# Performance work log

Hardware: AMD Instinct MI355X
Metric: run time of the kernel (lower is better)

The kernel has to match this reference:

```python
import jax, jax.numpy as jnp
import numpy as np

INPUT_SIZE = 1024
HIDDEN_SIZE = 1024
BATCH = 32
SEQ = 512


def setup_inputs() -> dict:
    key = jax.random.key(0)
    ks = jax.random.split(key, 20)
    stdv = 1.0 / np.sqrt(HIDDEN_SIZE)

    def u(k, shape):
        return jax.random.uniform(k, shape, jnp.float32, -stdv, stdv)

    inp = {
        'inputs': jax.random.normal(ks[0], (BATCH, SEQ, INPUT_SIZE), jnp.float32),
        'h0': jax.random.normal(ks[1], (1, BATCH, HIDDEN_SIZE), jnp.float32),
        'c0': jax.random.normal(ks[2], (1, BATCH, HIDDEN_SIZE), jnp.float32),
    }
    names = ['ii', 'hi', 'if_', 'hf', 'io', 'ho', 'ig', 'hg']
    kidx = 3
    for n in names:
        in_dim = INPUT_SIZE if n[0] == 'i' and n not in ('hi', 'hf', 'ho', 'hg') else HIDDEN_SIZE
        inp['w_' + n] = u(ks[kidx], (HIDDEN_SIZE, in_dim)); kidx += 1
        inp['b_' + n] = u(ks[kidx], (HIDDEN_SIZE, 1)); kidx += 1
    return inp


def _gate(x, h0s, w_i, b_i, w_h, b_h):
    # x: [B,T,I]; h0s: [B,H]; w_i: [H,I]; w_h: [H,H]; biases [H,1]
    z = (jnp.einsum('bti,hi->bth', x, w_i)
         + (h0s @ w_h.T)[:, None, :]
         + b_i[:, 0] + b_h[:, 0])
    return z


def reference(inputs, h0, c0,
              w_ii, b_ii, w_hi, b_hi,
              w_if_, b_if_, w_hf, b_hf,
              w_io, b_io, w_ho, b_ho,
              w_ig, b_ig, w_hg, b_hg):
    # Faithful to source: h_t/c_t are NEVER updated inside the time loop
    # (original code omits the reassignment), so all timesteps use the
    # initial state -> fully vectorizable over T.
    h0s = h0[0]  # [B,H]
    c0s = c0[0]  # [B,H]
    i = jax.nn.sigmoid(_gate(inputs, h0s, w_ii, b_ii, w_hi, b_hi))
    f = jax.nn.sigmoid(_gate(inputs, h0s, w_if_, b_if_, w_hf, b_hf))
    g = jnp.tanh(_gate(inputs, h0s, w_ig, b_ig, w_hg, b_hg))
    o = jax.nn.sigmoid(_gate(inputs, h0s, w_io, b_io, w_ho, b_ho))
    c_next = f * c0s[:, None, :] + i * g          # [B,T,H]
    h_next = o * jnp.tanh(c_next)                 # [B,T,H]
    hidden_seq = jnp.transpose(h_next, (1, 0, 2))  # [T,B,H] (torch cat over dim 0)
    h_last = hidden_seq[-1][None]                  # [1,B,H]
    c_last = c_next[:, -1][None]                   # [1,B,H]
    return hidden_seq, h_last, c_last
```

## Files before the change

kernel.cpp:

```cpp
#include <hip/hip_runtime.h>
#include <hip/hip_bf16.h>

#define HSEQ 16777216
#define NH 1024

typedef __attribute__((ext_vector_type(8))) short bf16x8;
typedef __attribute__((ext_vector_type(4))) float f32x4;

__device__ __forceinline__ unsigned short f2bf(float f) {
  unsigned u = __builtin_bit_cast(unsigned, f);
  u += 0x7fffu + ((u >> 16) & 1u);
  return (unsigned short)(u >> 16);
}

__global__ __launch_bounds__(256) void cvt_all(
    const float* __restrict__ x,
    const float* __restrict__ wi, const float* __restrict__ wf,
    const float* __restrict__ wo, const float* __restrict__ wg,
    unsigned short* __restrict__ xb, unsigned short* __restrict__ wb) {
  int bid = blockIdx.x;
  const float* src; unsigned short* dst; int base, iters;
  if (bid < 2048) {
    src = x; dst = xb; base = bid * 8192; iters = 8;
  } else {
    int g = bid - 2048; int ws = g >> 8; int blk = g & 255;
    src = (ws == 0) ? wi : (ws == 1) ? wf : (ws == 2) ? wo : wg;
    dst = wb + ws * 1048576; base = blk * 4096; iters = 4;
  }
  int t = threadIdx.x;
  for (int i = 0; i < iters; ++i) {
    int idx = base + i * 1024 + t * 4;
    float4 v = *reinterpret_cast<const float4*>(src + idx);
    ushort4 o;
    o.x = f2bf(v.x); o.y = f2bf(v.y); o.z = f2bf(v.z); o.w = f2bf(v.w);
    *reinterpret_cast<ushort4*>(dst + idx) = o;
  }
}

__global__ __launch_bounds__(256) void hz_kernel(
    const float* __restrict__ h0,
    const float* __restrict__ wh_i, const float* __restrict__ wh_f,
    const float* __restrict__ wh_o, const float* __restrict__ wh_g,
    const float* __restrict__ bi_i, const float* __restrict__ bh_i,
    const float* __restrict__ bi_f, const float* __restrict__ bh_f,
    const float* __restrict__ bi_o, const float* __restrict__ bh_o,
    const float* __restrict__ bi_g, const float* __restrict__ bh_g,
    float* __restrict__ hz) {
  __shared__ float ws[8 * 1024];
  int g = blockIdx.x >> 7;
  int hb = blockIdx.x & 127;
  const float* wh = (g == 0) ? wh_i : (g == 1) ? wh_f : (g == 2) ? wh_o : wh_g;
  const float* bi = (g == 0) ? bi_i : (g == 1) ? bi_f : (g == 2) ? bi_o : bi_g;
  const float* bh = (g == 0) ? bh_i : (g == 1) ? bh_f : (g == 2) ? bh_o : bh_g;
  int tid = threadIdx.x;
  const float4* wsrc = reinterpret_cast<const float4*>(wh + hb * 8 * 1024);
  float4* wdst = reinterpret_cast<float4*>(ws);
  for (int i = tid; i < 2048; i += 256) wdst[i] = wsrc[i];
  __syncthreads();
  int b = tid & 31;
  int hh = tid >> 5;
  const float4* hv = reinterpret_cast<const float4*>(h0 + b * NH);
  const float4* wv = reinterpret_cast<const float4*>(ws + hh * NH);
  float acc = 0.f;
  for (int k = 0; k < 256; ++k) {
    float4 a = hv[k], w4 = wv[k];
    acc += a.x * w4.x + a.y * w4.y + a.z * w4.z + a.w * w4.w;
  }
  int h = hb * 8 + hh;
  hz[g * (32 * NH) + b * NH + h] = acc + bi[h] + bh[h];
}

__device__ __forceinline__ void load_lds16(const void* gsrc, void* lds) {
  __builtin_amdgcn_global_load_lds(
      (const __attribute__((address_space(1))) unsigned int*)gsrc,
      (__attribute__((address_space(3))) unsigned int*)lds, 16, 0, 0);
}

__global__ __launch_bounds__(512, 2) void lstm_gemm8(
    const unsigned short* __restrict__ xb,
    const unsigned short* __restrict__ wb,
    const float* __restrict__ hz,
    const float* __restrict__ c0,
    float* __restrict__ out) {
  __shared__ unsigned short As[2][16384];
  __shared__ unsigned short Bs[2][16384];

  const int bid0 = blockIdx.x;
  const int bid = (bid0 & 7) * 128 + (bid0 >> 3);
  const int ht = bid & 15;
  const int mt = bid >> 4;
  const int mBase = mt * 256;
  const int hBase = ht * 64;

  const int tid = threadIdx.x;
  const int lane = tid & 63;
  const int w = tid >> 6;
  const int wr = w >> 2;
  const int wc = w & 3;
  const int laneLow = lane & 15;
  const int lane4 = lane >> 4;
  const int lx = lane & 7;

  const int sRow = w * 8 + (lane >> 3);
  const int sCol = ((lane & 7) ^ (lane >> 3)) * 8;

#define STAGE_A(buf, kt, h)                                                        \
  do {                                                                             \
    int k0_ = (kt) * 64;                                                           \
    _Pragma("unroll") for (int r_ = 0; r_ < 2; ++r_) {                             \
      load_lds16(xb + (size_t)(mBase + (h) * 128 + r_ * 64 + sRow) * 1024 + k0_ + sCol, \
                 &As[buf][(h) * 8192 + r_ * 4096 + w * 512]);                      \
    }                                                                              \
  } while (0)

#define STAGE_B(buf, kt, h)                                                        \
  do {                                                                             \
    int k0_ = (kt) * 64;                                                           \
    _Pragma("unroll") for (int r_ = 0; r_ < 2; ++r_) {                             \
      load_lds16(wb + (size_t)((h) * 2 + r_) * 1048576 +                           \
                     (size_t)(hBase + sRow) * 1024 + k0_ + sCol,                   \
                 &Bs[buf][(h) * 8192 + r_ * 4096 + w * 512]);                      \
    }                                                                              \
  } while (0)

#define LDA(buf, mh)                                                               \
  do {                                                                             \
    _Pragma("unroll") for (int mi = 0; mi < 4; ++mi)                               \
    _Pragma("unroll") for (int kk = 0; kk < 2; ++kk) {                             \
      int row_ = wr * 128 + (mh) * 64 + mi * 16 + laneLow;                         \
      int slot_ = (kk * 4 + lane4) ^ lx;                                           \
      af[mi][kk] = *reinterpret_cast<const bf16x8*>(&As[buf][row_ * 64 + slot_ * 8]); \
    }                                                                              \
  } while (0)

#define LDB(buf, qh)                                                               \
  do {                                                                             \
    _Pragma("unroll") for (int q = 0; q < 2; ++q)                                  \
    _Pragma("unroll") for (int kk = 0; kk < 2; ++kk) {                             \
      int row_ = ((qh) * 2 + q) * 64 + wc * 16 + laneLow;                          \
      int slot_ = (kk * 4 + lane4) ^ lx;                                           \
      bq[q][kk] = *reinterpret_cast<const bf16x8*>(&Bs[buf][row_ * 64 + slot_ * 8]); \
    }                                                                              \
  } while (0)

#define DO_MFMA(MH, QH)                                                            \
  do {                                                                             \
    __builtin_amdgcn_s_setprio(1);                                                 \
    _Pragma("unroll") for (int mi = 0; mi < 4; ++mi)                               \
    _Pragma("unroll") for (int q = 0; q < 2; ++q)                                  \
    _Pragma("unroll") for (int kk = 0; kk < 2; ++kk)                               \
      acc[(MH) * 4 + mi][(QH) * 2 + q] = __builtin_amdgcn_mfma_f32_16x16x32_bf16(  \
          af[mi][kk], bq[q][kk], acc[(MH) * 4 + mi][(QH) * 2 + q], 0, 0, 0);       \
    __builtin_amdgcn_s_setprio(0);                                                 \
  } while (0)

#define BARRIER __builtin_amdgcn_s_barrier()
#define WAIT_LGKM0 asm volatile("s_waitcnt lgkmcnt(0)" ::: "memory")

  f32x4 acc[8][4];
#pragma unroll
  for (int i = 0; i < 8; ++i)
#pragma unroll
    for (int j = 0; j < 4; ++j) acc[i][j] = (f32x4){0.f, 0.f, 0.f, 0.f};

  STAGE_B(0, 0, 0); STAGE_B(0, 0, 1);
  STAGE_A(0, 0, 0); STAGE_A(0, 0, 1);
  STAGE_B(1, 1, 0);
  asm volatile("s_waitcnt vmcnt(2)" ::: "memory");
  BARRIER;

  bf16x8 af[4][2], bq[2][2];

  for (int it = 0; it < 8; ++it) {
    const int t1 = 2 * it + 1;
    const int t2 = (2 * it + 2 > 15) ? 15 : 2 * it + 2;
    const int t3 = (2 * it + 3 > 15) ? 15 : 2 * it + 3;

    LDA(0, 0); LDB(0, 0);
    STAGE_B(1, t1, 1); STAGE_A(1, t1, 0);
    BARRIER; WAIT_LGKM0; DO_MFMA(0, 0); BARRIER;

    LDB(0, 1);
    STAGE_A(1, t1, 1);
    BARRIER; WAIT_LGKM0; DO_MFMA(0, 1); BARRIER;

    LDA(0, 1); LDB(0, 0);
    BARRIER; WAIT_LGKM0; DO_MFMA(1, 0); BARRIER;

    LDB(0, 1);
    STAGE_B(0, t2, 0); STAGE_A(0, t2, 0);
    asm volatile("s_waitcnt vmcnt(4)" ::: "memory");
    BARRIER; WAIT_LGKM0; DO_MFMA(1, 1); BARRIER;

    LDA(1, 0); LDB(1, 0);
    STAGE_B(0, t2, 1);
    BARRIER; WAIT_LGKM0; DO_MFMA(0, 0); BARRIER;

    LDB(1, 1);
    STAGE_A(0, t2, 1);
    BARRIER; WAIT_LGKM0; DO_MFMA(0, 1); BARRIER;

    LDA(1, 1); LDB(1, 0);
    BARRIER; WAIT_LGKM0; DO_MFMA(1, 0); BARRIER;

    LDB(1, 1);
    STAGE_B(1, t3, 0);
    asm volatile("s_waitcnt vmcnt(2)" ::: "memory");
    BARRIER; WAIT_LGKM0; DO_MFMA(1, 1); BARRIER;
  }

  const int b = mBase >> 9;
  const int h = hBase + wc * 16 + laneLow;
  float hzv[4];
#pragma unroll
  for (int g = 0; g < 4; ++g) hzv[g] = hz[g * 32768 + b * NH + h];
  const float c0v = c0[b * NH + h];
#pragma unroll
  for (int mi16 = 0; mi16 < 8; ++mi16) {
#pragma unroll
    for (int r = 0; r < 4; ++r) {
      int m = mBase + wr * 128 + mi16 * 16 + lane4 * 4 + r;
      int t = m & 511;
      float zi = acc[mi16][0][r] + hzv[0];
      float zf = acc[mi16][1][r] + hzv[1];
      float zo = acc[mi16][2][r] + hzv[2];
      float zg = acc[mi16][3][r] + hzv[3];
      float iv = 1.f / (1.f + __expf(-zi));
      float fv = 1.f / (1.f + __expf(-zf));
      float ov = 1.f / (1.f + __expf(-zo));
      float gv = tanhf(zg);
      float cv = fv * c0v + iv * gv;
      float hval = ov * tanhf(cv);
      out[(size_t)t * 32768 + b * NH + h] = hval;
      if (t == 511) {
        out[HSEQ + b * NH + h] = hval;
        out[HSEQ + 32768 + b * NH + h] = cv;
      }
    }
  }
}

extern "C" void kernel_launch(void* const* d_in, const int* in_sizes, int n_in,
                              void* d_out, int out_size, void* d_ws, size_t ws_size,
                              hipStream_t stream) {
  const float* x    = (const float*)d_in[0];
  const float* h0   = (const float*)d_in[1];
  const float* c0   = (const float*)d_in[2];
  const float* w_ii = (const float*)d_in[3];
  const float* b_ii = (const float*)d_in[4];
  const float* w_hi = (const float*)d_in[5];
  const float* b_hi = (const float*)d_in[6];
  const float* w_if = (const float*)d_in[7];
  const float* b_if = (const float*)d_in[8];
  const float* w_hf = (const float*)d_in[9];
  const float* b_hf = (const float*)d_in[10];
  const float* w_io = (const float*)d_in[11];
  const float* b_io = (const float*)d_in[12];
  const float* w_ho = (const float*)d_in[13];
  const float* b_ho = (const float*)d_in[14];
  const float* w_ig = (const float*)d_in[15];
  const float* b_ig = (const float*)d_in[16];
  const float* w_hg = (const float*)d_in[17];
  const float* b_hg = (const float*)d_in[18];

  unsigned short* xb = (unsigned short*)d_ws;
  unsigned short* wb = xb + 16777216;
  float* hz = (float*)(wb + 4 * 1048576);
  float* out = (float*)d_out;

  hipLaunchKernelGGL(cvt_all, dim3(3072), dim3(256), 0, stream,
                     x, w_ii, w_if, w_io, w_ig, xb, wb);
  hipLaunchKernelGGL(hz_kernel, dim3(512), dim3(256), 0, stream, h0,
                     w_hi, w_hf, w_ho, w_hg,
                     b_ii, b_hi, b_if, b_hf, b_io, b_ho, b_ig, b_hg, hz);
  hipLaunchKernelGGL(lstm_gemm8, dim3(1024), dim3(512), 0, stream, xb, wb, hz, c0, out);
}
```

Before: 257.4 us.

## Double-buffer LDS fragment registers to overlap loads with MFMA in GEMM loop

Restructures the main K loop so LDS-to-register fragment loads for the next MFMA block go into alternate register sets (afX/afY, bqA/bqB) while the current MFMA block runs. This removes the per-phase lgkmcnt(0) waits and halves the barriers. Global staging addresses are also precomputed as 32-bit offsets to cut address arithmetic. The cost is extra VGPR pressure and a more fragile hand-ordered schedule of buffer reuse across barriers.

```diff
diff --git a/kernel.cpp b/kernel.cpp
--- a/kernel.cpp
+++ b/kernel.cpp
@@ -103,59 +103,58 @@
 
   const int sRow = w * 8 + (lane >> 3);
   const int sCol = ((lane & 7) ^ (lane >> 3)) * 8;
+  const unsigned aStage = (unsigned)((mBase + sRow) * 1024 + sCol);
+  const unsigned bStage = (unsigned)((hBase + sRow) * 1024 + sCol);
 
 #define STAGE_A(buf, kt, h)                                                        \
   do {                                                                             \
-    int k0_ = (kt) * 64;                                                           \
     _Pragma("unroll") for (int r_ = 0; r_ < 2; ++r_) {                             \
-      load_lds16(xb + (size_t)(mBase + (h) * 128 + r_ * 64 + sRow) * 1024 + k0_ + sCol, \
+      load_lds16(xb + aStage + (unsigned)(((h) * 128 + r_ * 64) * 1024 + (kt) * 64), \
                  &As[buf][(h) * 8192 + r_ * 4096 + w * 512]);                      \
     }                                                                              \
   } while (0)
 
 #define STAGE_B(buf, kt, h)                                                        \
   do {                                                                             \
-    int k0_ = (kt) * 64;                                                           \
     _Pragma("unroll") for (int r_ = 0; r_ < 2; ++r_) {                             \
-      load_lds16(wb + (size_t)((h) * 2 + r_) * 1048576 +                           \
-                     (size_t)(hBase + sRow) * 1024 + k0_ + sCol,                   \
+      load_lds16(wb + bStage + (unsigned)(((h) * 2 + r_) * 1048576 + (kt) * 64),   \
                  &Bs[buf][(h) * 8192 + r_ * 4096 + w * 512]);                      \
     }                                                                              \
   } while (0)
 
-#define LDA(buf, mh)                                                               \
+#define LDA(dst, buf, mh)                                                          \
   do {                                                                             \
     _Pragma("unroll") for (int mi = 0; mi < 4; ++mi)                               \
     _Pragma("unroll") for (int kk = 0; kk < 2; ++kk) {                             \
       int row_ = wr * 128 + (mh) * 64 + mi * 16 + laneLow;                         \
       int slot_ = (kk * 4 + lane4) ^ lx;                                           \
-      af[mi][kk] = *reinterpret_cast<const bf16x8*>(&As[buf][row_ * 64 + slot_ * 8]); \
-    }                                                                              \
-  } while (0)
-
-#define LDB(buf, qh)                                                               \
+      dst[mi][kk] = *reinterpret_cast<const bf16x8*>(&As[buf][row_ * 64 + slot_ * 8]); \
+    }                                                                              \
+  } while (0)
+
+#define LDB(dst, buf, qh)                                                          \
   do {                                                                             \
     _Pragma("unroll") for (int q = 0; q < 2; ++q)                                  \
     _Pragma("unroll") for (int kk = 0; kk < 2; ++kk) {                             \
       int row_ = ((qh) * 2 + q) * 64 + wc * 16 + laneLow;                          \
       int slot_ = (kk * 4 + lane4) ^ lx;                                           \
-      bq[q][kk] = *reinterpret_cast<const bf16x8*>(&Bs[buf][row_ * 64 + slot_ * 8]); \
-    }                                                                              \
-  } while (0)
-
-#define DO_MFMA(MH, QH)                                                            \
+      dst[q][kk] = *reinterpret_cast<const bf16x8*>(&Bs[buf][row_ * 64 + slot_ * 8]); \
+    }                                                                              \
+  } while (0)
+
+#define MFMA16(A, B, MH, QH)                                                       \
   do {                                                                             \
     __builtin_amdgcn_s_setprio(1);                                                 \
     _Pragma("unroll") for (int mi = 0; mi < 4; ++mi)                               \
     _Pragma("unroll") for (int q = 0; q < 2; ++q)                                  \
     _Pragma("unroll") for (int kk = 0; kk < 2; ++kk)                               \
       acc[(MH) * 4 + mi][(QH) * 2 + q] = __builtin_amdgcn_mfma_f32_16x16x32_bf16(  \
-          af[mi][kk], bq[q][kk], acc[(MH) * 4 + mi][(QH) * 2 + q], 0, 0, 0);       \
+          A[mi][kk], B[q][kk], acc[(MH) * 4 + mi][(QH) * 2 + q], 0, 0, 0);         \
     __builtin_amdgcn_s_setprio(0);                                                 \
   } while (0)
 
-#define BARRIER __builtin_amdgcn_s_barrier()
-#define WAIT_LGKM0 asm volatile("s_waitcnt lgkmcnt(0)" ::: "memory")
+#define BAR __builtin_amdgcn_s_barrier()
+#define VM(n) asm volatile("s_waitcnt vmcnt(" #n ")" ::: "memory")
 
   f32x4 acc[8][4];
 #pragma unroll
@@ -163,50 +162,61 @@
 #pragma unroll
     for (int j = 0; j < 4; ++j) acc[i][j] = (f32x4){0.f, 0.f, 0.f, 0.f};
 
-  STAGE_B(0, 0, 0); STAGE_B(0, 0, 1);
-  STAGE_A(0, 0, 0); STAGE_A(0, 0, 1);
-  STAGE_B(1, 1, 0);
-  asm volatile("s_waitcnt vmcnt(2)" ::: "memory");
-  BARRIER;
-
-  bf16x8 af[4][2], bq[2][2];
+  bf16x8 afX[4][2], afY[4][2], bqA[2][2], bqB[2][2];
+
+  STAGE_B(0, 0, 0); STAGE_B(0, 0, 1); STAGE_A(0, 0, 0); STAGE_A(0, 0, 1);
+  STAGE_B(1, 1, 0); STAGE_B(1, 1, 1); STAGE_A(1, 1, 0);
+  VM(0);
+  BAR;
+  LDB(bqA, 0, 0);
+  LDA(afX, 0, 0);
 
   for (int it = 0; it < 8; ++it) {
-    const int t1 = 2 * it + 1;
-    const int t2 = (2 * it + 2 > 15) ? 15 : 2 * it + 2;
-    const int t3 = (2 * it + 3 > 15) ? 15 : 2 * it + 3;
-
-    LDA(0, 0); LDB(0, 0);
-    STAGE_B(1, t1, 1); STAGE_A(1, t1, 0);
-    BARRIER; WAIT_LGKM0; DO_MFMA(0, 0); BARRIER;
-
-    LDB(0, 1);
-    STAGE_A(1, t1, 1);
-    BARRIER; WAIT_LGKM0; DO_MFMA(0, 1); BARRIER;
-
-    LDA(0, 1); LDB(0, 0);
-    BARRIER; WAIT_LGKM0; DO_MFMA(1, 0); BARRIER;
-
-    LDB(0, 1);
-    STAGE_B(0, t2, 0); STAGE_A(0, t2, 0);
-    asm volatile("s_waitcnt vmcnt(4)" ::: "memory");
-    BARRIER; WAIT_LGKM0; DO_MFMA(1, 1); BARRIER;
-
-    LDA(1, 0); LDB(1, 0);
-    STAGE_B(0, t2, 1);
-    BARRIER; WAIT_LGKM0; DO_MFMA(0, 0); BARRIER;
-
-    LDB(1, 1);
-    STAGE_A(0, t2, 1);
-    BARRIER; WAIT_LGKM0; DO_MFMA(0, 1); BARRIER;
-
-    LDA(1, 1); LDB(1, 0);
-    BARRIER; WAIT_LGKM0; DO_MFMA(1, 0); BARRIER;
-
-    LDB(1, 1);
-    STAGE_B(1, t3, 0);
-    asm volatile("s_waitcnt vmcnt(2)" ::: "memory");
-    BARRIER; WAIT_LGKM0; DO_MFMA(1, 1); BARRIER;
+    const int tOdd = 2 * it + 1;
+    const int tA2 = (2 * it + 2 > 15) ? 15 : 2 * it + 2;
+    const int tB2 = (2 * it + 3 > 15) ? 15 : 2 * it + 3;
+
+    LDB(bqB, 0, 1);
+    STAGE_A(1, tOdd, 1);
+    MFMA16(afX, bqA, 0, 0);
+    BAR;
+
+    LDA(afY, 0, 1);
+    STAGE_B(0, tA2, 0);
+    MFMA16(afX, bqB, 0, 1);
+    BAR;
+
+    STAGE_B(0, tA2, 1);
+    MFMA16(afY, bqB, 1, 1);
+    VM(4);
+    BAR;
+
+    LDB(bqB, 1, 0);
+    LDA(afX, 1, 0);
+    STAGE_A(0, tA2, 0);
+    MFMA16(afY, bqA, 1, 0);
+    BAR;
+
+    LDB(bqA, 1, 1);
+    STAGE_A(0, tA2, 1);
+    MFMA16(afX, bqB, 0, 0);
+    BAR;
+
+    LDA(afY, 1, 1);
+    STAGE_B(1, tB2, 0);
+    MFMA16(afX, bqA, 0, 1);
+    BAR;
+
+    STAGE_B(1, tB2, 1);
+    MFMA16(afY, bqA, 1, 1);
+    VM(4);
+    BAR;
+
+    LDB(bqA, 0, 0);
+    LDA(afX, 0, 0);
+    STAGE_A(1, tB2, 0);
+    MFMA16(afY, bqB, 1, 0);
+    BAR;
   }
 
   const int b = mBase >> 9;
```

Measured after the change: 262.0 us. About the same (+1.8%).
